# Kernel tuning notes

Measured on AMD Instinct MI355X. Metric: run time of the kernel, lower is better.

Reference implementation:

```python
import jax, jax.numpy as jnp
import numpy as np

DIM = 256
HEADS = 8
HD = DIM // HEADS        # head_dim = 32
WS = 8                   # window_size (Wh = Ww = 8)
NEXP = 8                 # num_experts
HID = 128                # attr_hidden_size (router hidden)
SCALE = HD ** -0.5


def _window_partition(x, ws):
    # (B, H, W, C) -> (B * H//ws * W//ws, ws, ws, C)
    B, H, W, C = x.shape
    x = x.reshape(B, H // ws, ws, W // ws, ws, C)
    return x.transpose(0, 1, 3, 2, 4, 5).reshape(-1, ws, ws, C)


def _window_reverse(w, ws, B, H, W):
    # inverse of _window_partition
    C = w.shape[-1]
    x = w.reshape(B, H // ws, W // ws, ws, ws, C)
    return x.transpose(0, 1, 3, 2, 4, 5).reshape(B, H, W, C)


def _rope2(x):
    # 2D rotary embedding over a window: x (B*, Wh, Ww, d).
    # First d/2 channels rotated by row position, last d/2 by column position.
    B, Wh, Ww, d = x.shape
    d2 = d // 2

    def angles(L, dd):
        inv = 1.0 / (10000.0 ** (jnp.arange(0, dd, 2, dtype=jnp.float32) / dd))
        return jnp.arange(L, dtype=jnp.float32)[:, None] * inv[None, :]  # (L, dd//2)

    def rotate(v, ang, bshape):
        # v: (B, Wh, Ww, dd) pairs interleaved; ang broadcast as bshape
        p = v.reshape(*v.shape[:-1], -1, 2)
        c = jnp.cos(ang).reshape(bshape)
        s = jnp.sin(ang).reshape(bshape)
        o0 = p[..., 0] * c - p[..., 1] * s
        o1 = p[..., 0] * s + p[..., 1] * c
        return jnp.stack([o0, o1], axis=-1).reshape(v.shape)

    ah = angles(Wh, d2)  # (Wh, d2//2)
    aw = angles(Ww, d2)  # (Ww, d2//2)
    xh = rotate(x[..., :d2], ah, (1, Wh, 1, d2 // 2))
    xw = rotate(x[..., d2:], aw, (1, 1, Ww, d2 // 2))
    return jnp.concatenate([xh, xw], axis=-1)


def _moe_linear(xf, routes, w, b):
    # Top-1 dispatch: per-expert dense GEMM, masked select (jit-safe, static shapes).
    # xf: (T, in), routes: (T,) int, w: (E, out, in), b: (E, out)
    out = jnp.zeros((xf.shape[0], w.shape[1]), xf.dtype)
    for i in range(w.shape[0]):
        y = xf @ w[i].T + b[i]
        out = jnp.where((routes == i)[:, None], y, out)
    return out


def setup_inputs() -> dict:
    key = jax.random.key(0)
    ks = jax.random.split(key, 8)
    sc = 0.02
    return {
        "x": jax.random.normal(ks[0], (8, 64, 64, DIM), jnp.float32),
        "router_w1": jax.random.normal(ks[1], (HID, DIM), jnp.float32) * sc,
        "router_b1": jnp.zeros((HID,), jnp.float32),
        "router_w2": jax.random.normal(ks[2], (NEXP, HID), jnp.float32) * sc,
        "router_b2": jnp.zeros((NEXP,), jnp.float32),
        "qkv_w": jax.random.normal(ks[3], (NEXP, 3 * DIM, DIM), jnp.float32) * sc,
        "qkv_b": jnp.zeros((NEXP, 3 * DIM), jnp.float32),
        "proj_w": jax.random.normal(ks[4], (NEXP, DIM, DIM), jnp.float32) * sc,
        "proj_b": jnp.zeros((NEXP, DIM), jnp.float32),
    }


def reference(x, router_w1, router_b1, router_w2, router_b2,
              qkv_w, qkv_b, proj_w, proj_b):
    Bs, H, W, C = x.shape
    xf = x.reshape(-1, C)  # (T, C), T = Bs*H*W

    # --- Top-1 router (eval mode: no noise, no token dropping) ---
    h = jax.nn.relu(xf @ router_w1.T + router_b1)
    router_logits = h @ router_w2.T + router_b2          # (T, E)
    router_probs = jax.nn.softmax(router_logits, axis=-1)
    route_prob_max = jnp.max(router_probs, axis=-1)       # (T,)
    routes = jnp.argmax(router_probs, axis=-1)            # (T,)

    # --- per-expert QKV projection (grouped dispatch) ---
    qkv = _moe_linear(xf, routes, qkv_w, qkv_b)           # (T, 3C)
    qkv = qkv.reshape(Bs, H, W, 3 * C)

    # --- window partition (shift=0, dilated=1 -> no roll, mask=None) ---
    qw = _window_partition(qkv, WS).reshape(-1, WS * WS, 3 * C)
    B_, N, _ = qw.shape
    qkv5 = qw.reshape(B_, N, 3, HEADS, HD).transpose(2, 0, 3, 1, 4)  # (3,B_,h,N,hd)
    q, k, v = qkv5[0], qkv5[1], qkv5[2]

    # --- RoPE on q, k over the 2D window ---
    q = _rope2(q.reshape(-1, WS, WS, HD)).reshape(B_, HEADS, N, HD)
    k = _rope2(k.reshape(-1, WS, WS, HD)).reshape(B_, HEADS, N, HD)

    # --- windowed attention (moe_mask is all zeros in eval: no drops) ---
    attn = jax.nn.softmax((q * SCALE) @ k.swapaxes(-2, -1), axis=-1)  # (B_,h,N,N)
    out = (attn @ v).swapaxes(1, 2).reshape(B_, N, C)

    # --- window reverse ---
    out = _window_reverse(out.reshape(-1, WS, WS, C), WS, Bs, H, W)

    # --- per-expert output projection + Switch-style prob scaling ---
    of = _moe_linear(out.reshape(-1, C), routes, proj_w, proj_b)
    of = of * route_prob_max[:, None]
    return of.reshape(Bs, H, W, C)
```

## Files before the change

### kernel.cpp

```cpp
#include <hip/hip_runtime.h>
#include <hip/hip_bf16.h>

typedef unsigned short u16;
typedef unsigned int u32;
typedef __attribute__((ext_vector_type(8))) short short8;
typedef __attribute__((ext_vector_type(4))) float f32x4;

#define T_TOK 32768
#define SCALE_ATT 0.17677669529663687f

__device__ __forceinline__ u16 f2bf(float f){
  u32 u = __float_as_uint(f);
  u32 r = u + 0x7fffu + ((u >> 16) & 1u);
  return (u16)(r >> 16);
}
__device__ __forceinline__ float bf2f(u16 h){
  return __uint_as_float(((u32)h) << 16);
}

__device__ __forceinline__ int xcd_swz(int flat, int nwg){
  return (flat & 7) * (nwg >> 3) + (flat >> 3);
}

__global__ __launch_bounds__(256) void k_prep(
    const float* __restrict__ qkvw, u16* __restrict__ qw_bf,
    const float* __restrict__ projw, u16* __restrict__ pw_bf,
    const float* __restrict__ rw1, u16* __restrict__ w1h, u16* __restrict__ w1l,
    int* __restrict__ sorted, int* __restrict__ counts, int* __restrict__ cursors)
{
  int b = blockIdx.x, tid = threadIdx.x;
  if (b < 1536){
    int i = b * 256 + tid;
    float4 v = ((const float4*)qkvw)[i];
    ushort4 o;
    o.x = f2bf(v.x); o.y = f2bf(v.y); o.z = f2bf(v.z); o.w = f2bf(v.w);
    ((ushort4*)qw_bf)[i] = o;
  } else if (b < 2048){
    int i = (b - 1536) * 256 + tid;
    float4 v = ((const float4*)projw)[i];
    ushort4 o;
    o.x = f2bf(v.x); o.y = f2bf(v.y); o.z = f2bf(v.z); o.w = f2bf(v.w);
    ((ushort4*)pw_bf)[i] = o;
  } else if (b < 2176){
    int i = (b - 2048) * 256 + tid;
    float v = rw1[i];
    u16 h = f2bf(v);
    w1h[i] = h;
    w1l[i] = f2bf(v - bf2f(h));
  } else if (b < 2209){
    int i = (b - 2176) * 256 + tid;
    int4 m1 = {-1, -1, -1, -1};
    ((int4*)sorted)[i] = m1;
  } else {
    if (tid < 8){ counts[tid] = 0; cursors[tid] = 0; }
  }
}

__global__ __launch_bounds__(256) void k_router(
    const float* __restrict__ x, const u16* __restrict__ w1h, const u16* __restrict__ w1l,
    const float* __restrict__ b1, const float* __restrict__ w2, const float* __restrict__ b2,
    int* __restrict__ routes, float* __restrict__ pmax, int* __restrict__ counts,
    u16* __restrict__ x_bf)
{
  __shared__ __align__(16) char smem[64*132*4];
  u16* Ah = (u16*)smem;
  u16* Al = Ah + 2560;
  u16* Bh = Al + 2560;
  u16* Bl = Bh + 5120;
  float* Hs = (float*)smem;
  __shared__ int lhist[8];

  int tid = threadIdx.x;
  int t0 = blockIdx.x * 64;
  int wv = tid >> 6, lane = tid & 63, quad = lane >> 4, l16 = lane & 15;
  if (tid < 8) lhist[tid] = 0;

  int arow = tid >> 2, acg = tid & 3;
  int brow = tid >> 1, bhalf = tid & 1;

  f32x4 acc[4][2];
  #pragma unroll
  for (int i = 0; i < 4; ++i)
    #pragma unroll
    for (int j = 0; j < 2; ++j)
      #pragma unroll
      for (int rr = 0; rr < 4; ++rr) acc[i][j][rr] = 0.f;

  for (int kt = 0; kt < 8; ++kt){
    const float* gx = x + (size_t)(t0 + arow) * 256 + kt * 32 + acg * 8;
    float4 v0 = *(const float4*)gx;
    float4 v1 = *(const float4*)(gx + 4);
    ushort4 h0, h1, l0, l1;
    h0.x = f2bf(v0.x); h0.y = f2bf(v0.y); h0.z = f2bf(v0.z); h0.w = f2bf(v0.w);
    h1.x = f2bf(v1.x); h1.y = f2bf(v1.y); h1.z = f2bf(v1.z); h1.w = f2bf(v1.w);
    l0.x = f2bf(v0.x - bf2f(h0.x)); l0.y = f2bf(v0.y - bf2f(h0.y));
    l0.z = f2bf(v0.z - bf2f(h0.z)); l0.w = f2bf(v0.w - bf2f(h0.w));
    l1.x = f2bf(v1.x - bf2f(h1.x)); l1.y = f2bf(v1.y - bf2f(h1.y));
    l1.z = f2bf(v1.z - bf2f(h1.z)); l1.w = f2bf(v1.w - bf2f(h1.w));
    u16* gxb = x_bf + (size_t)(t0 + arow) * 256 + kt * 32 + acg * 8;
    *(ushort4*)gxb = h0; *(ushort4*)(gxb + 4) = h1;
    const u16* gwh = w1h + (size_t)brow * 256 + kt * 32 + bhalf * 16;
    const u16* gwl = w1l + (size_t)brow * 256 + kt * 32 + bhalf * 16;
    uint4 wh0 = *(const uint4*)gwh;
    uint4 wh1 = *(const uint4*)(gwh + 8);
    uint4 wl0 = *(const uint4*)gwl;
    uint4 wl1 = *(const uint4*)(gwl + 8);
    __syncthreads();
    *(ushort4*)&Ah[arow*40 + acg*8    ] = h0;
    *(ushort4*)&Ah[arow*40 + acg*8 + 4] = h1;
    *(ushort4*)&Al[arow*40 + acg*8    ] = l0;
    *(ushort4*)&Al[arow*40 + acg*8 + 4] = l1;
    *(uint4*)&Bh[brow*40 + bhalf*16    ] = wh0;
    *(uint4*)&Bh[brow*40 + bhalf*16 + 8] = wh1;
    *(uint4*)&Bl[brow*40 + bhalf*16    ] = wl0;
    *(uint4*)&Bl[brow*40 + bhalf*16 + 8] = wl1;
    __syncthreads();
    short8 ah[4], al[4], bhf[2], blf[2];
    #pragma unroll
    for (int i = 0; i < 4; ++i){
      ah[i] = *(const short8*)&Ah[(i*16 + l16)*40 + quad*8];
      al[i] = *(const short8*)&Al[(i*16 + l16)*40 + quad*8];
    }
    #pragma unroll
    for (int j = 0; j < 2; ++j){
      bhf[j] = *(const short8*)&Bh[(wv*32 + j*16 + l16)*40 + quad*8];
      blf[j] = *(const short8*)&Bl[(wv*32 + j*16 + l16)*40 + quad*8];
    }
    #pragma unroll
    for (int i = 0; i < 4; ++i)
      #pragma unroll
      for (int j = 0; j < 2; ++j){
        acc[i][j] = __builtin_amdgcn_mfma_f32_16x16x32_bf16(ah[i], bhf[j], acc[i][j], 0, 0, 0);
        acc[i][j] = __builtin_amdgcn_mfma_f32_16x16x32_bf16(ah[i], blf[j], acc[i][j], 0, 0, 0);
        acc[i][j] = __builtin_amdgcn_mfma_f32_16x16x32_bf16(al[i], bhf[j], acc[i][j], 0, 0, 0);
      }
  }
  __syncthreads();

  #pragma unroll
  for (int i = 0; i < 4; ++i)
    #pragma unroll
    for (int j = 0; j < 2; ++j){
      int col = wv*32 + j*16 + l16;
      float bb = b1[col];
      #pragma unroll
      for (int rr = 0; rr < 4; ++rr){
        float h = acc[i][j][rr] + bb;
        Hs[(i*16 + quad*4 + rr)*132 + col] = h > 0.f ? h : 0.f;
      }
    }
  __syncthreads();

  #pragma unroll
  for (int pass = 0; pass < 2; ++pass){
    int mtok = (tid >> 3) + pass * 32;
    int e = tid & 7;
    const float4* w2r = (const float4*)(w2 + e * 128);
    float l = b2[e];
    #pragma unroll
    for (int k4 = 0; k4 < 32; ++k4){
      float4 w = w2r[k4];
      int k = k4 * 4;
      l = fmaf(Hs[mtok*132+k  ], w.x, l);
      l = fmaf(Hs[mtok*132+k+1], w.y, l);
      l = fmaf(Hs[mtok*132+k+2], w.z, l);
      l = fmaf(Hs[mtok*132+k+3], w.w, l);
    }
    float mv = l; int mi = e;
    #pragma unroll
    for (int off = 1; off < 8; off <<= 1){
      float ov = __shfl_xor(mv, off, 64);
      int   oi = __shfl_xor(mi, off, 64);
      if (ov > mv || (ov == mv && oi < mi)){ mv = ov; mi = oi; }
    }
    float sum = expf(l - mv);
    #pragma unroll
    for (int off = 1; off < 8; off <<= 1) sum += __shfl_xor(sum, off, 64);
    if (e == 0){
      int t = t0 + mtok;
      routes[t] = mi;
      pmax[t] = 1.0f / sum;
      atomicAdd(&lhist[mi], 1);
    }
  }
  __syncthreads();
  if (tid < 8 && lhist[tid] > 0) atomicAdd(&counts[tid], lhist[tid]);
}

__global__ __launch_bounds__(256) void k_scatter(
    const int* __restrict__ routes, const int* __restrict__ counts,
    int* __restrict__ cursors, int* __restrict__ sorted, int* __restrict__ rank,
    int* __restrict__ offs)
{
  __shared__ int lc[8], lb[8], so[9];
  int tid = threadIdx.x;
  if (tid == 0){
    int o = 0; so[0] = 0;
    #pragma unroll
    for (int e = 0; e < 8; ++e){ o += ((counts[e] + 127) >> 7) << 7; so[e+1] = o; }
  }
  if (tid < 8) lc[tid] = 0;
  __syncthreads();
  int t = blockIdx.x * 256 + tid;
  int e = routes[t];
  int rl = atomicAdd(&lc[e], 1);
  __syncthreads();
  if (tid < 8 && lc[tid] > 0) lb[tid] = atomicAdd(&cursors[tid], lc[tid]);
  __syncthreads();
  int pos = so[e] + lb[e] + rl;
  sorted[pos] = t;
  rank[t] = pos;
  if (blockIdx.x == 0 && tid < 9) offs[tid] = so[tid];
}

#define ASTR 56
template<int NOUT, bool PROJ, int NB, int NWG>
__global__ __launch_bounds__(256) void k_gemm(
    const u16* __restrict__ A, const u16* __restrict__ W,
    const float* __restrict__ bias, const int* __restrict__ sidx,
    const int* __restrict__ offs, const float* __restrict__ pmax,
    u16* __restrict__ outb, float* __restrict__ outf)
{
  __shared__ __align__(16) u16 As[128 * ASTR];
  __shared__ __align__(16) u16 Bs[128 * ASTR];
  int tid = threadIdx.x;
  int flat = blockIdx.y * NB + blockIdx.x;
  int logical = xcd_swz(flat, NWG);
  int m0 = (logical / NB) * 128;
  int n0 = (logical % NB) * 128;
  int total = offs[8];
  if (m0 >= total) return;
  int e = 0;
  #pragma unroll
  for (int i = 1; i < 8; ++i) if (m0 >= offs[i]) e = i;

  int wv = tid >> 6, lane = tid & 63, quad = lane >> 4, l16 = lane & 15;
  int wrow = (wv >> 1) * 64, wcol = (wv & 1) * 64;

  int row0 = tid >> 2, c0 = tid & 3;
  const u16 *aptr0, *aptr1;
  if (PROJ){
    aptr0 = A + (size_t)(m0 + row0) * 256 + c0 * 8;
    aptr1 = aptr0 + (size_t)64 * 256;
  } else {
    int tA0 = sidx[m0 + row0];      if (tA0 < 0) tA0 = 0;
    int tA1 = sidx[m0 + row0 + 64]; if (tA1 < 0) tA1 = 0;
    aptr0 = A + (size_t)tA0 * 256 + c0 * 8;
    aptr1 = A + (size_t)tA1 * 256 + c0 * 8;
  }
  int pc = (row0 >> 4) + (row0 & 15) * 4;
  const u16* bptr0 = W + ((size_t)e * NOUT + n0 + pc) * 256 + c0 * 8;
  const u16* bptr1 = W + ((size_t)e * NOUT + n0 + 64 + pc) * 256 + c0 * 8;

  f32x4 acc[4][4];
  #pragma unroll
  for (int i = 0; i < 4; ++i)
    #pragma unroll
    for (int j = 0; j < 4; ++j)
      #pragma unroll
      for (int r = 0; r < 4; ++r) acc[i][j][r] = 0.f;

  uint4 a0 = *(const uint4*)aptr0, a1 = *(const uint4*)aptr1;
  uint4 b0 = *(const uint4*)bptr0, b1 = *(const uint4*)bptr1;

  for (int kt = 0; kt < 8; ++kt){
    __syncthreads();
    *(uint4*)&As[ row0      *ASTR + c0*8] = a0;
    *(uint4*)&As[(row0 + 64)*ASTR + c0*8] = a1;
    *(uint4*)&Bs[ row0      *ASTR + c0*8] = b0;
    *(uint4*)&Bs[(row0 + 64)*ASTR + c0*8] = b1;
    __syncthreads();
    if (kt < 7){
      a0 = *(const uint4*)(aptr0 + (kt+1)*32);
      a1 = *(const uint4*)(aptr1 + (kt+1)*32);
      b0 = *(const uint4*)(bptr0 + (kt+1)*32);
      b1 = *(const uint4*)(bptr1 + (kt+1)*32);
    }
    short8 af[4], bfv[4];
    #pragma unroll
    for (int i = 0; i < 4; ++i)
      af[i] = *(const short8*)&As[(wrow + i*16 + l16)*ASTR + quad*8];
    #pragma unroll
    for (int j = 0; j < 4; ++j)
      bfv[j] = *(const short8*)&Bs[(wcol + j*16 + l16)*ASTR + quad*8];
    #pragma unroll
    for (int i = 0; i < 4; ++i)
      #pragma unroll
      for (int j = 0; j < 4; ++j)
        acc[i][j] = __builtin_amdgcn_mfma_f32_16x16x32_bf16(af[i], bfv[j], acc[i][j], 0, 0, 0);
  }

  float4 bj4 = *(const float4*)&bias[e*NOUT + n0 + wcol + l16*4];
  if (PROJ){
    #pragma unroll
    for (int i = 0; i < 4; ++i){
      #pragma unroll
      for (int ri = 0; ri < 4; ++ri){
        int row = wrow + i*16 + quad*4 + ri;
        int t = sidx[m0 + row];
        if (t < 0) continue;
        float pm = pmax[t];
        float4 ov;
        ov.x = (acc[i][0][ri] + bj4.x) * pm;
        ov.y = (acc[i][1][ri] + bj4.y) * pm;
        ov.z = (acc[i][2][ri] + bj4.z) * pm;
        ov.w = (acc[i][3][ri] + bj4.w) * pm;
        *(float4*)&outf[(size_t)t * NOUT + n0 + wcol + l16*4] = ov;
      }
    }
  } else {
    int col0 = n0 + wcol + l16*4;
    bool isqk = (col0 < 512);
    float inv0 = 0.f, inv1 = 0.f;
    float qsc = (col0 < 256) ? SCALE_ATT : 1.0f;
    if (isqk){
      int p0 = (col0 & 15) >> 1;
      inv0 = __expf(-1.1512925465f * (float)p0);
      inv1 = inv0 * 0.31622776601683794f;
    }
    #pragma unroll
    for (int i = 0; i < 4; ++i){
      #pragma unroll
      for (int ri = 0; ri < 4; ++ri){
        int row = wrow + i*16 + quad*4 + ri;
        int t = sidx[m0 + row];
        if (t < 0) continue;
        float vx = acc[i][0][ri] + bj4.x;
        float vy = acc[i][1][ri] + bj4.y;
        float vz = acc[i][2][ri] + bj4.z;
        float vw = acc[i][3][ri] + bj4.w;
        if (isqk){
          float pos = (float)((col0 & 16) ? (t & 7) : ((t >> 6) & 7));
          float a0r = pos * inv0, a1r = pos * inv1;
          float s0, c0s, s1, c1s;
          __sincosf(a0r, &s0, &c0s);
          __sincosf(a1r, &s1, &c1s);
          float r0 = (vx*c0s - vy*s0) * qsc;
          float r1 = (vx*s0 + vy*c0s) * qsc;
          float r2 = (vz*c1s - vw*s1) * qsc;
          float r3 = (vz*s1 + vw*c1s) * qsc;
          vx = r0; vy = r1; vz = r2; vw = r3;
        }
        uint2 ov;
        ov.x = (u32)f2bf(vx) | ((u32)f2bf(vy) << 16);
        ov.y = (u32)f2bf(vz) | ((u32)f2bf(vw) << 16);
        *(uint2*)&outb[(size_t)t * NOUT + n0 + wcol + l16*4] = ov;
      }
    }
  }
}

__global__ __launch_bounds__(64, 3) void k_attn(const u16* __restrict__ qkv,
                                                const int* __restrict__ rank,
                                                u16* __restrict__ attn_s)
{
  __shared__ __align__(16) u16 Ps[64*72];
  __shared__ __align__(16) u16 Vt[32*72];

  int lane = threadIdx.x;
  int quad = lane >> 4, l16 = lane & 15;
  int wh = xcd_swz(blockIdx.x, 4096);
  int win = wh >> 3, head = wh & 7;
  int b = win >> 6, wy = (win >> 3) & 7, wx = win & 7;
  int tb = b*4096 + wy*512 + wx*8;

  short8 qf[4], kf[4];
  #pragma unroll
  for (int i = 0; i < 4; ++i){
    int n = i*16 + l16;
    const u16* p = qkv + (size_t)(tb + (n>>3)*64 + (n&7)) * 768 + head*32 + quad*8;
    qf[i] = *(const short8*)p;
    kf[i] = *(const short8*)(p + 256);
  }
  int tn = tb + (lane>>3)*64 + (lane&7);
  const uint4* vb = (const uint4*)(qkv + (size_t)tn * 768 + 512 + head*32);
  uint4 va[4];
  #pragma unroll
  for (int i = 0; i < 4; ++i) va[i] = vb[i];

  f32x4 sa[4][4];
  #pragma unroll
  for (int i = 0; i < 4; ++i)
    #pragma unroll
    for (int j = 0; j < 4; ++j){
      #pragma unroll
      for (int rr = 0; rr < 4; ++rr) sa[i][j][rr] = 0.f;
      sa[i][j] = __builtin_amdgcn_mfma_f32_16x16x32_bf16(qf[i], kf[j], sa[i][j], 0, 0, 0);
    }

  f32x4 rs[4];
  #pragma unroll
  for (int i = 0; i < 4; ++i)
    #pragma unroll
    for (int rr = 0; rr < 4; ++rr){
      float e0 = __expf(sa[i][0][rr]);
      float e1 = __expf(sa[i][1][rr]);
      float e2 = __expf(sa[i][2][rr]);
      float e3 = __expf(sa[i][3][rr]);
      rs[i][rr] = (e0 + e1) + (e2 + e3);
      uint2 pk;
      pk.x = (u32)f2bf(e0) | ((u32)f2bf(e1) << 16);
      pk.y = (u32)f2bf(e2) | ((u32)f2bf(e3) << 16);
      *(uint2*)&Ps[(i*16 + quad*4 + rr)*72 + l16*4] = pk;
    }
  #pragma unroll
  for (int i = 0; i < 4; ++i)
    #pragma unroll
    for (int rr = 0; rr < 4; ++rr){
      #pragma unroll
      for (int off = 1; off < 16; off <<= 1)
        rs[i][rr] += __shfl_xor(rs[i][rr], off, 64);
    }

  u32* vu = (u32*)va;
  int pn = l16 * 4 + quad;
  #pragma unroll
  for (int d2 = 0; d2 < 16; ++d2){
    Vt[(2*d2  )*72 + pn] = (u16)(vu[d2] & 0xffff);
    Vt[(2*d2+1)*72 + pn] = (u16)(vu[d2] >> 16);
  }

  f32x4 oa[4][2];
  #pragma unroll
  for (int i = 0; i < 4; ++i)
    #pragma unroll
    for (int rr = 0; rr < 4; ++rr){ oa[i][0][rr] = 0.f; oa[i][1][rr] = 0.f; }
  #pragma unroll
  for (int ks = 0; ks < 2; ++ks){
    short8 vf0 = *(const short8*)&Vt[(     l16)*72 + ks*32 + quad*8];
    short8 vf1 = *(const short8*)&Vt[(16 + l16)*72 + ks*32 + quad*8];
    #pragma unroll
    for (int i = 0; i < 4; ++i){
      short8 pf = *(const short8*)&Ps[(i*16 + l16)*72 + ks*32 + quad*8];
      oa[i][0] = __builtin_amdgcn_mfma_f32_16x16x32_bf16(pf, vf0, oa[i][0], 0, 0, 0);
      oa[i][1] = __builtin_amdgcn_mfma_f32_16x16x32_bf16(pf, vf1, oa[i][1], 0, 0, 0);
    }
  }

  #pragma unroll
  for (int i = 0; i < 4; ++i)
    #pragma unroll
    for (int rr = 0; rr < 4; ++rr){
      float inv = __builtin_amdgcn_rcpf(rs[i][rr]);
      int m = i*16 + quad*4 + rr;
      int tm = tb + (m >> 3) * 64 + (m & 7);
      int pos = rank[tm];
      u16* op = attn_s + (size_t)pos * 256 + head * 32 + l16;
      op[0]  = f2bf(oa[i][0][rr] * inv);
      op[16] = f2bf(oa[i][1][rr] * inv);
    }
}

extern "C" void kernel_launch(void* const* d_in, const int* in_sizes, int n_in,
                              void* d_out, int out_size, void* d_ws, size_t ws_size,
                              hipStream_t stream){
  const float* x     = (const float*)d_in[0];
  const float* rw1   = (const float*)d_in[1];
  const float* rb1   = (const float*)d_in[2];
  const float* rw2   = (const float*)d_in[3];
  const float* rb2   = (const float*)d_in[4];
  const float* qkvw  = (const float*)d_in[5];
  const float* qkvb  = (const float*)d_in[6];
  const float* projw = (const float*)d_in[7];
  const float* projb = (const float*)d_in[8];
  float* out = (float*)d_out;

  char* ws = (char*)d_ws;
  u16*   x_bf    = (u16*)(ws);
  u16*   qkv_bf  = (u16*)(ws + 16777216);
  u16*   w1h     = (u16*)(ws + 67108864);
  u16*   w1l     = w1h + 32768;
  u16*   attn_s  = (u16*)(ws + 67108864);
  u16*   qw_bf   = (u16*)(ws + 84410368);
  u16*   pw_bf   = (u16*)(ws + 87556096);
  int*   routes  = (int*)(ws + 88604672);
  float* pmaxp   = (float*)(ws + 88735744);
  int*   sorted  = (int*)(ws + 88866816);
  int*   rank    = (int*)(ws + 89001984);
  int*   counts  = (int*)(ws + 89133056);
  int*   cursors = (int*)(ws + 89133056 + 32);
  int*   offs    = (int*)(ws + 89133056 + 64);

  k_prep<<<2210, 256, 0, stream>>>(qkvw, qw_bf, projw, pw_bf, rw1, w1h, w1l,
                                   sorted, counts, cursors);
  k_router<<<512, 256, 0, stream>>>(x, w1h, w1l, rb1, rw2, rb2, routes, pmaxp, counts, x_bf);
  k_scatter<<<128, 256, 0, stream>>>(routes, counts, cursors, sorted, rank, offs);
  k_gemm<768, false, 6, 1584><<<dim3(6, 264), 256, 0, stream>>>(
      x_bf, qw_bf, qkvb, sorted, offs, nullptr, qkv_bf, nullptr);
  k_attn<<<4096, 64, 0, stream>>>(qkv_bf, rank, attn_s);
  k_gemm<256, true, 2, 528><<<dim3(2, 264), 256, 0, stream>>>(
      attn_s, pw_bf, projb, sorted, offs, pmaxp, nullptr, out);
}
```

Measured before the change: 197.4 us.

## Write QKV in head-major window-contiguous layout and prefetch ranks in attention

The QKV GEMM epilogue now scatters its bf16 output into a [q/k/v][head][window][token][32] layout instead of token-major rows of 768. Each attention block can then read its Q, K and V tiles as contiguous 4 KB chunks rather than strided 64-byte pieces. The block-to-(head, window) mapping is reordered to match, and the rank lookups are hoisted to the start of the kernel so their latency overlaps the loads. In exchange, the GEMM epilogue writes become scattered 8-byte stores, which may coalesce less well.

```diff
diff --git a/kernel.cpp b/kernel.cpp
--- a/kernel.cpp
+++ b/kernel.cpp
@@ -318,6 +318,10 @@
       inv0 = __expf(-1.1512925465f * (float)p0);
       inv1 = inv0 * 0.31622776601683794f;
     }
+    int sel  = col0 >> 8;
+    int head = (col0 >> 5) & 7;
+    int ch   = col0 & 31;
+    size_t hb = ((size_t)(sel * 8 + head) * 512) * 2048 + ch;
     #pragma unroll
     for (int i = 0; i < 4; ++i){
       #pragma unroll
@@ -341,10 +345,12 @@
           float r3 = (vz*s1 + vw*c1s) * qsc;
           vx = r0; vy = r1; vz = r2; vw = r3;
         }
+        int win = (t >> 12) * 64 + ((t >> 9) & 7) * 8 + ((t >> 3) & 7);
+        int n   = ((t >> 6) & 7) * 8 + (t & 7);
         uint2 ov;
         ov.x = (u32)f2bf(vx) | ((u32)f2bf(vy) << 16);
         ov.y = (u32)f2bf(vz) | ((u32)f2bf(vw) << 16);
-        *(uint2*)&outb[(size_t)t * NOUT + n0 + wcol + l16*4] = ov;
+        *(uint2*)&outb[hb + (size_t)win * 2048 + n * 32] = ov;
       }
     }
   }
@@ -360,23 +366,33 @@
   int lane = threadIdx.x;
   int quad = lane >> 4, l16 = lane & 15;
   int wh = xcd_swz(blockIdx.x, 4096);
-  int win = wh >> 3, head = wh & 7;
+  int head = wh >> 9, win = wh & 511;
   int b = win >> 6, wy = (win >> 3) & 7, wx = win & 7;
   int tb = b*4096 + wy*512 + wx*8;
 
+  const u16* qbase = qkv + (size_t)(head * 512 + win) * 2048;
+  const u16* kbase = qbase + (size_t)8 * 512 * 2048;
+  const u16* vbase = qbase + (size_t)16 * 512 * 2048;
+
+  int rk[4][4];
+  #pragma unroll
+  for (int i = 0; i < 4; ++i)
+    #pragma unroll
+    for (int rr = 0; rr < 4; ++rr){
+      int m = i*16 + quad*4 + rr;
+      rk[i][rr] = rank[tb + (m >> 3) * 64 + (m & 7)];
+    }
+
   short8 qf[4], kf[4];
   #pragma unroll
   for (int i = 0; i < 4; ++i){
-    int n = i*16 + l16;
-    const u16* p = qkv + (size_t)(tb + (n>>3)*64 + (n&7)) * 768 + head*32 + quad*8;
-    qf[i] = *(const short8*)p;
-    kf[i] = *(const short8*)(p + 256);
-  }
-  int tn = tb + (lane>>3)*64 + (lane&7);
-  const uint4* vb = (const uint4*)(qkv + (size_t)tn * 768 + 512 + head*32);
+    qf[i] = *(const short8*)(qbase + (i*16 + l16)*32 + quad*8);
+    kf[i] = *(const short8*)(kbase + (i*16 + l16)*32 + quad*8);
+  }
   uint4 va[4];
   #pragma unroll
-  for (int i = 0; i < 4; ++i) va[i] = vb[i];
+  for (int h = 0; h < 4; ++h)
+    va[h] = *(const uint4*)(vbase + h*512 + l16*32 + quad*8);
 
   f32x4 sa[4][4];
   #pragma unroll
@@ -413,11 +429,15 @@
     }
 
   u32* vu = (u32*)va;
-  int pn = l16 * 4 + quad;
-  #pragma unroll
-  for (int d2 = 0; d2 < 16; ++d2){
-    Vt[(2*d2  )*72 + pn] = (u16)(vu[d2] & 0xffff);
-    Vt[(2*d2+1)*72 + pn] = (u16)(vu[d2] >> 16);
+  #pragma unroll
+  for (int h = 0; h < 4; ++h){
+    int pn = l16 * 4 + h;
+    #pragma unroll
+    for (int w = 0; w < 4; ++w){
+      u32 vv = vu[h*4 + w];
+      Vt[(quad*8 + 2*w    )*72 + pn] = (u16)(vv & 0xffff);
+      Vt[(quad*8 + 2*w + 1)*72 + pn] = (u16)(vv >> 16);
+    }
   }
 
   f32x4 oa[4][2];
@@ -442,9 +462,7 @@
     #pragma unroll
     for (int rr = 0; rr < 4; ++rr){
       float inv = __builtin_amdgcn_rcpf(rs[i][rr]);
-      int m = i*16 + quad*4 + rr;
-      int tm = tb + (m >> 3) * 64 + (m & 7);
-      int pos = rank[tm];
+      int pos = rk[i][rr];
       u16* op = attn_s + (size_t)pos * 256 + head * 32 + l16;
       op[0]  = f2bf(oa[i][0][rr] * inv);
       op[16] = f2bf(oa[i][1][rr] * inv);
```

New measurement: 196.0 us. About the same (-0.7%).
